# Optimization experiments

Hardware: AMD Instinct MI355X
Metric: run time of the kernel (lower is better)

The kernel has to match this reference:

```python
import math
import jax, jax.numpy as jnp
import numpy as np

B, V, D, H, DE, DFF = 2, 2048, 1024, 16, 256, 4096
DK = D // H


def setup_inputs() -> dict:
    key = jax.random.key(0)
    ks = jax.random.split(key, 24)
    n = lambda k, shape, s=0.02: (jax.random.normal(k, shape, jnp.float32) * s)
    z = lambda *shape: jnp.zeros(shape, jnp.float32)
    return {
        'x': jax.random.normal(ks[0], (B, V, D), jnp.float32),
        'e_node': jax.random.normal(ks[1], (B, V, DE), jnp.float32),
        'conn': jax.random.uniform(ks[2], (B, V, V), jnp.float32),
        'ln1_g': jnp.ones((D,), jnp.float32), 'ln1_b': z(D),
        'f1w1': n(ks[3], (DE, 2 * D)), 'f1b1': z(2 * D),
        'f1w2': n(ks[4], (2 * D, 2 * D)), 'f1b2': z(2 * D),
        'wq': n(ks[5], (D, D)), 'bq': z(D),
        'wk': n(ks[6], (D, D)), 'bk': z(D),
        'wv': n(ks[7], (D, D)), 'bv': z(D),
        'wp': n(ks[8], (D, D)), 'bp': z(D),
        'ln2_g': jnp.ones((D,), jnp.float32), 'ln2_b': z(D),
        'f2w1': n(ks[9], (DE, 2 * D)), 'f2b1': z(2 * D),
        'f2w2': n(ks[10], (2 * D, 2 * D)), 'f2b2': z(2 * D),
        'ffw1': n(ks[11], (D, DFF)), 'ffb1': z(DFF),
        'ffw2': n(ks[12], (DFF, D)), 'ffb2': z(D),
    }


def _ln(x, g, b):
    m = x.mean(-1, keepdims=True)
    v = ((x - m) ** 2).mean(-1, keepdims=True)
    return (x - m) / jnp.sqrt(v + 1e-5) * g + b


def _film(e, w1, b1, w2, b2):
    h = jax.nn.gelu(e @ w1 + b1, approximate=False)  # torch F.gelu default = exact erf
    gb = h @ w2 + b2
    return jnp.split(gb, 2, axis=-1)  # gamma, beta


def reference(x, e_node, conn, ln1_g, ln1_b, f1w1, f1b1, f1w2, f1b2,
              wq, bq, wk, bk, wv, bv, wp, bp, ln2_g, ln2_b,
              f2w1, f2b1, f2w2, f2b2, ffw1, ffb1, ffw2, ffb2):
    b, v, d = x.shape
    # Pre-norm + FiLM 1
    y = _ln(x, ln1_g, ln1_b)
    g1, be1 = _film(e_node, f1w1, f1b1, f1w2, f1b2)
    y = y * (1.0 + g1) + be1
    # Multi-head attention with additive log(conn) mask
    heads = lambda t: t.reshape(b, v, H, DK).transpose(0, 2, 1, 3)  # [B,h,V,dk]
    Q = heads(y @ wq + bq)
    K = heads(y @ wk + bk)
    Vv = heads(y @ wv + bv)
    logits = jnp.einsum('bhqd,bhkd->bhqk', Q, K) / math.sqrt(DK)
    log_mask = jnp.log(jnp.clip(conn, 0.0, 1.0) + 1e-6)[:, None]  # [B,1,V,V]
    s = logits + log_mask
    s = s - s.max(-1, keepdims=True)
    a = jnp.exp(s)
    a = a / (a.sum(-1, keepdims=True) + 1e-8)
    o = jnp.einsum('bhqk,bhkd->bhqd', a, Vv)
    o = o.transpose(0, 2, 1, 3).reshape(b, v, d)
    x = x + (o @ wp + bp)
    # Pre-norm + FiLM 2 + FFN
    y2 = _ln(x, ln2_g, ln2_b)
    g2, be2 = _film(e_node, f2w1, f2b1, f2w2, f2b2)
    y2 = y2 * (1.0 + g2) + be2
    y2 = jax.nn.gelu(y2 @ ffw1 + ffb1, approximate=False) @ ffw2 + ffb2
    return x + y2
```

## Files before the change

kernel.cpp:

```cpp
#include <hip/hip_runtime.h>
#include <math.h>
#include <stdint.h>

#define B_   2
#define V_   2048
#define D_   1024
#define H_   16
#define DK_  64
#define DE_  256
#define DFF_ 4096
#define M_   (B_*V_)
#define D2_  (2*D_)
#define D3_  (3*D_)

typedef unsigned short u16;
typedef unsigned int   u32;
typedef __bf16 bf16x8 __attribute__((ext_vector_type(8)));
typedef u16    u16x8  __attribute__((ext_vector_type(8)));
typedef u16    u16x4  __attribute__((ext_vector_type(4)));
typedef float  f32x4  __attribute__((ext_vector_type(4)));
typedef u32    u32x2  __attribute__((ext_vector_type(2)));
typedef u32    u32x4  __attribute__((ext_vector_type(4)));

__device__ __forceinline__ float bf2f(u16 u) {
    union { unsigned int i; float f; } z; z.i = ((unsigned int)u) << 16; return z.f;
}
__device__ __forceinline__ u16 f2bf(float f) {
    union { float f; unsigned int i; } z; z.f = f;
    unsigned int x = z.i;
    return (u16)((x + 0x7fffu + ((x >> 16) & 1u)) >> 16);
}
__device__ __forceinline__ float gelu_erf(float v) {
    return 0.5f * v * (1.0f + erff(v * 0.70710678118654752f));
}
__device__ __forceinline__ float ldv(const float* p) { return *p; }
__device__ __forceinline__ float ldv(const u16* p)   { return bf2f(*p); }
__device__ __forceinline__ void  stv(float* p, float v) { *p = v; }
__device__ __forceinline__ void  stv(u16* p,   float v) { *p = f2bf(v); }

__device__ __forceinline__ void gload16(const u16* g, u16* lds)
{
    __builtin_amdgcn_global_load_lds(
        (const __attribute__((address_space(1))) void*)g,
        (__attribute__((address_space(3))) void*)(uintptr_t)lds,
        16, 0, 0);
}

__global__ void convT_k(const float* __restrict__ W, u16* __restrict__ Wt, int K, int N)
{
    __shared__ float tile[32][33];
    const int n0 = blockIdx.x * 32, k0 = blockIdx.y * 32;
    const int tx = threadIdx.x, ty = threadIdx.y;
    #pragma unroll
    for (int j = 0; j < 4; ++j)
        tile[ty * 4 + j][tx] = W[(size_t)(k0 + ty * 4 + j) * N + n0 + tx];
    __syncthreads();
    #pragma unroll
    for (int j = 0; j < 4; ++j)
        Wt[(size_t)(n0 + ty * 4 + j) * K + k0 + tx] = f2bf(tile[tx][ty * 4 + j]);
}

__global__ void conv_k(const float* __restrict__ X, u16* __restrict__ Y)
{
    const int i = (blockIdx.x * 256 + threadIdx.x) * 4;
    f32x4 v = *reinterpret_cast<const f32x4*>(X + i);
    u16x4 o;
    #pragma unroll
    for (int j = 0; j < 4; ++j) o[j] = f2bf(v[j]);
    *reinterpret_cast<u16x4*>(Y + i) = o;
}

__global__ void lmask_k(const float* __restrict__ conn, u16* __restrict__ Lm)
{
    const size_t i = ((size_t)blockIdx.x * 256 + threadIdx.x) * 8;
    f32x4 a = *reinterpret_cast<const f32x4*>(conn + i);
    f32x4 b = *reinterpret_cast<const f32x4*>(conn + i + 4);
    u16x8 o;
    #pragma unroll
    for (int j = 0; j < 4; ++j) {
        o[j]     = f2bf(__logf(fminf(fmaxf(a[j], 0.f), 1.f) + 1e-6f));
        o[j + 4] = f2bf(__logf(fminf(fmaxf(b[j], 0.f), 1.f) + 1e-6f));
    }
    *reinterpret_cast<u16x8*>(Lm + i) = o;
}

__global__ void qkvbias_k(const float* __restrict__ bq, const float* __restrict__ bk,
                          const float* __restrict__ bv, float* __restrict__ o)
{
    int i = blockIdx.x * 256 + threadIdx.x;
    o[i] = i < 1024 ? bq[i] : (i < 2048 ? bk[i - 1024] : bv[i - 2048]);
}

template<int EPI, typename TC, typename TRES>
__launch_bounds__(256)
__global__ void gemm_k(const u16* __restrict__ A, const u16* __restrict__ Wt,
                       const float* __restrict__ bias, const TRES* __restrict__ res,
                       TC* __restrict__ C, int M, int N, int K)
{
    __shared__ u16 As[128 * 64];
    __shared__ u16 Bs[128 * 64];

    const int tid  = threadIdx.x;
    const int lane = tid & 63;
    const int w    = tid >> 6;
    const int wm   = (w >> 1) * 64, wn = (w & 1) * 64;
    const int m0   = blockIdx.y * 128, n0 = blockIdx.x * 128;
    const int l15  = lane & 15, l4 = lane >> 4;

    int rr[4], cc[4];
    #pragma unroll
    for (int i = 0; i < 4; ++i) {
        rr[i] = w * 32 + i * 8 + (lane >> 3);
        cc[i] = (lane & 7) ^ (rr[i] & 7);
    }

    f32x4 acc[4][4] = {};

    for (int k0 = 0; k0 < K; k0 += 64) {
        if (k0) __syncthreads();
        #pragma unroll
        for (int i = 0; i < 4; ++i) {
            gload16(A  + (size_t)(m0 + rr[i]) * K + k0 + cc[i] * 8, &As[w * 2048 + i * 512]);
            gload16(Wt + (size_t)(n0 + rr[i]) * K + k0 + cc[i] * 8, &Bs[w * 2048 + i * 512]);
        }
        __syncthreads();

        #pragma unroll
        for (int kk = 0; kk < 2; ++kk) {
            bf16x8 a[4], b[4];
            #pragma unroll
            for (int mb = 0; mb < 4; ++mb) {
                int r  = wm + mb * 16 + l15;
                int ph = (kk * 4 + l4) ^ (r & 7);
                a[mb] = *reinterpret_cast<const bf16x8*>(&As[r * 64 + ph * 8]);
            }
            #pragma unroll
            for (int nb = 0; nb < 4; ++nb) {
                int r  = wn + nb * 16 + l15;
                int ph = (kk * 4 + l4) ^ (r & 7);
                b[nb] = *reinterpret_cast<const bf16x8*>(&Bs[r * 64 + ph * 8]);
            }
            #pragma unroll
            for (int mb = 0; mb < 4; ++mb)
                #pragma unroll
                for (int nb = 0; nb < 4; ++nb)
                    acc[mb][nb] = __builtin_amdgcn_mfma_f32_16x16x32_bf16(a[mb], b[nb], acc[mb][nb], 0, 0, 0);
        }
    }

    #pragma unroll
    for (int nb = 0; nb < 4; ++nb) {
        int col = n0 + wn + nb * 16 + l15;
        float bv = bias[col];
        #pragma unroll
        for (int mb = 0; mb < 4; ++mb) {
            #pragma unroll
            for (int i = 0; i < 4; ++i) {
                int row = m0 + wm + mb * 16 + l4 * 4 + i;
                float v = acc[mb][nb][i] + bv;
                if (EPI == 1) v = gelu_erf(v);
                if (EPI == 2) v += ldv(res + (size_t)row * N + col);
                stv(C + (size_t)row * N + col, v);
            }
        }
    }
}

template<typename TX>
__launch_bounds__(256)
__global__ void lnfilm_k(const TX* __restrict__ X, const u16* __restrict__ GB,
                         const float* __restrict__ g, const float* __restrict__ bb,
                         u16* __restrict__ Y)
{
    const int row = blockIdx.x;
    const int tid = threadIdx.x;
    const TX* xr = X + (size_t)row * D_;
    float xs[4], s = 0.f, sq = 0.f;
    #pragma unroll
    for (int j = 0; j < 4; ++j) {
        float v = ldv(xr + tid + j * 256);
        xs[j] = v; s += v; sq += v * v;
    }
    #pragma unroll
    for (int off = 32; off; off >>= 1) {
        s  += __shfl_xor(s, off);
        sq += __shfl_xor(sq, off);
    }
    __shared__ float rs[4], rq[4];
    const int w = tid >> 6;
    if ((tid & 63) == 0) { rs[w] = s; rq[w] = sq; }
    __syncthreads();
    s  = rs[0] + rs[1] + rs[2] + rs[3];
    sq = rq[0] + rq[1] + rq[2] + rq[3];
    const float mean = s * (1.0f / D_);
    const float var  = sq * (1.0f / D_) - mean * mean;
    const float rstd = rsqrtf(fmaxf(var, 0.f) + 1e-5f);
    const u16* gbr = GB + (size_t)row * D2_;
    #pragma unroll
    for (int j = 0; j < 4; ++j) {
        int d = tid + j * 256;
        float v = (xs[j] - mean) * rstd * g[d] + bb[d];
        v = v * (1.0f + bf2f(gbr[d])) + bf2f(gbr[D_ + d]);
        Y[(size_t)row * D_ + d] = f2bf(v);
    }
}

__launch_bounds__(256)
__global__ void attn_k(const u16* __restrict__ Q, const u16* __restrict__ K,
                       const u16* __restrict__ Vv, const u16* __restrict__ Lm,
                       u16* __restrict__ O, int ld)
{
    __shared__ u16 Ks[64 * 64];
    __shared__ u16 Vs[64 * 64];
    __shared__ u16 Lms[64 * 64];
    __shared__ u16 Ps[4 * 16 * 72];

    const int blk = blockIdx.x;
    const int qt  = blk & 31;
    const int h   = (blk >> 5) & 15;
    const int b   = blk >> 9;
    const int q0  = qt * 64;
    const int tid = threadIdx.x, lane = tid & 63, w = tid >> 6;
    const int l15 = lane & 15, l4 = lane >> 4;
    const size_t bV = (size_t)b * V_;

    const u16* qp = Q + (bV + q0 + w * 16 + l15) * ld + h * 64;
    bf16x8 qa[2];
    {
        u16x8 r0 = *reinterpret_cast<const u16x8*>(qp + l4 * 8);
        u16x8 r1 = *reinterpret_cast<const u16x8*>(qp + 32 + l4 * 8);
        u16x8 s0, s1;
        #pragma unroll
        for (int j = 0; j < 8; ++j) {
            s0[j] = f2bf(bf2f(r0[j]) * 0.125f);
            s1[j] = f2bf(bf2f(r1[j]) * 0.125f);
        }
        union { u16x8 u; bf16x8 h; } c0, c1;
        c0.u = s0; c1.u = s1;
        qa[0] = c0.h; qa[1] = c1.h;
    }

    const int rStage  = (lane >> 3);
    const int kSrcDk  = ((lane & 7) ^ (lane >> 3)) * 8;
    const int vK      = ((lane >> 5) << 2) + ((lane & 7) >> 1);
    const int vDk     = ((lane >> 3) & 3) * 16 + (lane & 1) * 8;
    const int lmSrc   = ((lane & 7) * 8) ^ ((((w << 1) + (lane >> 5)) & 3) * 16);
    const u32 vaddr   = (u32)(uintptr_t)&Vs[0] + (l4 << 10) + (l15 << 3);

    float lr[4] = {0.f, 0.f, 0.f, 0.f};
    f32x4 o[4] = {};

    for (int kt = 0; kt < V_ / 64; ++kt) {
        const int k0 = kt * 64;
        if (kt) __syncthreads();
        #pragma unroll
        for (int i = 0; i < 2; ++i) {
            int r = i * 32 + w * 8 + rStage;
            gload16(K  + (bV + k0 + r) * ld + h * 64 + kSrcDk,           &Ks[i * 2048 + w * 512]);
            int kv = i * 32 + w * 8 + vK;
            gload16(Vv + (bV + k0 + kv) * ld + h * 64 + vDk,             &Vs[i * 2048 + w * 512]);
            gload16(Lm + (bV + q0 + r) * (size_t)V_ + k0 + lmSrc,        &Lms[i * 2048 + w * 512]);
        }
        __syncthreads();

        f32x4 s[4];
        #pragma unroll
        for (int kb = 0; kb < 4; ++kb) {
            int row = (kb * 16 + l15) * 64;
            bf16x8 b0 = *reinterpret_cast<const bf16x8*>(&Ks[row + ((l4 ^ (l15 & 7)) * 8)]);
            bf16x8 b1 = *reinterpret_cast<const bf16x8*>(&Ks[row + (((l4 + 4) ^ (l15 & 7)) * 8)]);
            f32x4 z = {};
            z = __builtin_amdgcn_mfma_f32_16x16x32_bf16(qa[0], b0, z, 0, 0, 0);
            z = __builtin_amdgcn_mfma_f32_16x16x32_bf16(qa[1], b1, z, 0, 0, 0);
            s[kb] = z;
        }
        float rsum[4] = {0.f, 0.f, 0.f, 0.f};
        #pragma unroll
        for (int i = 0; i < 4; ++i) {
            int lrow = (w * 16 + l4 * 4 + i) * 64;
            #pragma unroll
            for (int kb = 0; kb < 4; ++kb) {
                float p = __expf(s[kb][i] + bf2f(Lms[lrow + ((kb ^ l4) * 16 + l15)]));
                rsum[i] += p;
                Ps[(w * 16 + l4 * 4 + i) * 72 + kb * 16 + l15] = f2bf(p);
            }
        }
        #pragma unroll
        for (int i = 0; i < 4; ++i) {
            float v = rsum[i];
            #pragma unroll
            for (int off = 8; off; off >>= 1) v += __shfl_xor(v, off, 16);
            lr[i] += v;
        }
        #pragma unroll
        for (int c2 = 0; c2 < 2; ++c2) {
            bf16x8 pa = *reinterpret_cast<const bf16x8*>(&Ps[(w * 16 + l15) * 72 + c2 * 32 + l4 * 8]);
            u32 a0 = vaddr + c2 * 4096;
            u32x2 t0, t1, t2, t3, t4, t5, t6, t7;
            asm volatile("ds_read_b64_tr_b16 %0, %1"            : "=v"(t0) : "v"(a0));
            asm volatile("ds_read_b64_tr_b16 %0, %1 offset:512" : "=v"(t1) : "v"(a0));
            asm volatile("ds_read_b64_tr_b16 %0, %1 offset:128" : "=v"(t2) : "v"(a0));
            asm volatile("ds_read_b64_tr_b16 %0, %1 offset:640" : "=v"(t3) : "v"(a0));
            asm volatile("ds_read_b64_tr_b16 %0, %1 offset:256" : "=v"(t4) : "v"(a0));
            asm volatile("ds_read_b64_tr_b16 %0, %1 offset:768" : "=v"(t5) : "v"(a0));
            asm volatile("ds_read_b64_tr_b16 %0, %1 offset:384" : "=v"(t6) : "v"(a0));
            asm volatile("ds_read_b64_tr_b16 %0, %1 offset:896" : "=v"(t7) : "v"(a0));
            asm volatile("s_waitcnt lgkmcnt(0)" ::: "memory");
            __builtin_amdgcn_sched_barrier(0);
            union { u32x4 u; bf16x8 h; } vb0, vb1, vb2, vb3;
            vb0.u = (u32x4){t0.x, t0.y, t1.x, t1.y};
            vb1.u = (u32x4){t2.x, t2.y, t3.x, t3.y};
            vb2.u = (u32x4){t4.x, t4.y, t5.x, t5.y};
            vb3.u = (u32x4){t6.x, t6.y, t7.x, t7.y};
            o[0] = __builtin_amdgcn_mfma_f32_16x16x32_bf16(pa, vb0.h, o[0], 0, 0, 0);
            o[1] = __builtin_amdgcn_mfma_f32_16x16x32_bf16(pa, vb1.h, o[1], 0, 0, 0);
            o[2] = __builtin_amdgcn_mfma_f32_16x16x32_bf16(pa, vb2.h, o[2], 0, 0, 0);
            o[3] = __builtin_amdgcn_mfma_f32_16x16x32_bf16(pa, vb3.h, o[3], 0, 0, 0);
        }
    }

    #pragma unroll
    for (int i = 0; i < 4; ++i) {
        float rcp = 1.0f / (lr[i] + 1e-8f);
        int q = q0 + w * 16 + l4 * 4 + i;
        u16* op = O + (bV + q) * D_ + h * 64;
        #pragma unroll
        for (int nb = 0; nb < 4; ++nb)
            op[nb * 16 + l15] = f2bf(o[nb][i] * rcp);
    }
}

extern "C" void kernel_launch(void* const* d_in, const int* in_sizes, int n_in,
                              void* d_out, int out_size, void* d_ws, size_t ws_size,
                              hipStream_t stream)
{
    (void)in_sizes; (void)n_in; (void)out_size; (void)ws_size;
    const float* x    = (const float*)d_in[0];
    const float* e    = (const float*)d_in[1];
    const float* conn = (const float*)d_in[2];
    const float* ln1g = (const float*)d_in[3];
    const float* ln1b = (const float*)d_in[4];
    const float* f1w1 = (const float*)d_in[5];
    const float* f1b1 = (const float*)d_in[6];
    const float* f1w2 = (const float*)d_in[7];
    const float* f1b2 = (const float*)d_in[8];
    const float* wq   = (const float*)d_in[9];
    const float* bq   = (const float*)d_in[10];
    const float* wk   = (const float*)d_in[11];
    const float* bk   = (const float*)d_in[12];
    const float* wv   = (const float*)d_in[13];
    const float* bv   = (const float*)d_in[14];
    const float* wp   = (const float*)d_in[15];
    const float* bp   = (const float*)d_in[16];
    const float* ln2g = (const float*)d_in[17];
    const float* ln2b = (const float*)d_in[18];
    const float* f2w1 = (const float*)d_in[19];
    const float* f2b1 = (const float*)d_in[20];
    const float* f2w2 = (const float*)d_in[21];
    const float* f2b2 = (const float*)d_in[22];
    const float* ffw1 = (const float*)d_in[23];
    const float* ffb1 = (const float*)d_in[24];
    const float* ffw2 = (const float*)d_in[25];
    const float* ffb2 = (const float*)d_in[26];
    float* out = (float*)d_out;

    char* ws = (char*)d_ws;
    const size_t MB = 1u << 20;
    u16*   Lm    = (u16*)(ws + 0);
    u16*   e_bf  = (u16*)(ws + 16 * MB);
    u16*   h     = (u16*)(ws + 18 * MB);
    u16*   wt2   = (u16*)(ws + 34 * MB);
    u16*   wt8   = (u16*)(ws + 36 * MB);
    u16*   gb    = (u16*)(ws + 44 * MB);
    u16*   y     = (u16*)(ws + 60 * MB);
    u16*   wqkvt = (u16*)(ws + 18 * MB);
    u16*   qkv   = (u16*)(ws + 24 * MB);
    float* qkvb  = (float*)(ws + 71 * MB);
    u16*   o     = (u16*)(ws + 48 * MB);
    u16*   xnew  = (u16*)(ws + 64 * MB);
    u16*   h2    = (u16*)(ws + 18 * MB);
    u16*   gb2   = (u16*)(ws + 44 * MB);
    u16*   y2    = (u16*)(ws + 0);
    u16*   ffw1t = (u16*)(ws + 8 * MB);
    u16*   t     = (u16*)(ws + 16 * MB);
    u16*   ffw2t = (u16*)(ws + 48 * MB);

    dim3 blk(256), tblk(32, 8);
    #define CONVT(W, WT, K, N) convT_k<<<dim3((N)/32, (K)/32), tblk, 0, stream>>>(W, WT, K, N)

    conv_k <<<(M_*DE_)/1024, blk, 0, stream>>>(e, e_bf);
    lmask_k<<<(B_*(size_t)V_*V_)/2048, blk, 0, stream>>>(conn, Lm);

    CONVT(f1w1, wt2, DE_, D2_);
    gemm_k<1, u16, u16><<<dim3(D2_/128, M_/128), blk, 0, stream>>>(e_bf, wt2, f1b1, (const u16*)nullptr, h, M_, D2_, DE_);
    CONVT(f1w2, wt8, D2_, D2_);
    gemm_k<0, u16, u16><<<dim3(D2_/128, M_/128), blk, 0, stream>>>(h, wt8, f1b2, (const u16*)nullptr, gb, M_, D2_, D2_);
    lnfilm_k<float><<<M_, blk, 0, stream>>>(x, gb, ln1g, ln1b, y);
    CONVT(wq, wqkvt,                 D_, D_);
    CONVT(wk, wqkvt + 1024 * 1024,   D_, D_);
    CONVT(wv, wqkvt + 2048 * 1024,   D_, D_);
    qkvbias_k<<<D3_/256, blk, 0, stream>>>(bq, bk, bv, qkvb);
    gemm_k<0, u16, u16><<<dim3(D3_/128, M_/128), blk, 0, stream>>>(y, wqkvt, qkvb, (const u16*)nullptr, qkv, M_, D3_, D_);
    attn_k<<<B_*H_*(V_/64), blk, 0, stream>>>(qkv, qkv + 1024, qkv + 2048, Lm, o, D3_);
    CONVT(wp, wt2, D_, D_);
    gemm_k<2, u16, float><<<dim3(D_/128, M_/128), blk, 0, stream>>>(o, wt2, bp, x, xnew, M_, D_, D_);
    CONVT(f2w1, wt2, DE_, D2_);
    gemm_k<1, u16, u16><<<dim3(D2_/128, M_/128), blk, 0, stream>>>(e_bf, wt2, f2b1, (const u16*)nullptr, h2, M_, D2_, DE_);
    CONVT(f2w2, wt8, D2_, D2_);
    gemm_k<0, u16, u16><<<dim3(D2_/128, M_/128), blk, 0, stream>>>(h2, wt8, f2b2, (const u16*)nullptr, gb2, M_, D2_, D2_);
    lnfilm_k<u16><<<M_, blk, 0, stream>>>(xnew, gb2, ln2g, ln2b, y2);
    CONVT(ffw1, ffw1t, D_, DFF_);
    gemm_k<1, u16, u16><<<dim3(DFF_/128, M_/128), blk, 0, stream>>>(y2, ffw1t, ffb1, (const u16*)nullptr, t, M_, DFF_, D_);
    CONVT(ffw2, ffw2t, DFF_, D_);
    gemm_k<2, float, u16><<<dim3(D_/128, M_/128), blk, 0, stream>>>(t, ffw2t, ffb2, xnew, out, M_, D_, DFF_);
    #undef CONVT
}
```

Baseline: 449.2 us.

## Transpose QK MFMA output, vectorize mask/P LDS traffic, use exp2 softmax

The attention kernel swaps the MFMA operands so each lane holds four consecutive keys of one query row. This lets the log-mask be read as one 4-element vector and the probabilities be written as packed bf16 pairs, instead of scalar LDS accesses. The mask is now stored in log2 form and the softmax uses raw v_exp_f32 with a LOG2E FMA, replacing __expf. The row-sum shuffles move out of the key loop into a single reduction at the end, which adds a cross-lane gather to map sums back to the output layout.

```diff
diff --git a/kernel.cpp b/kernel.cpp
--- a/kernel.cpp
+++ b/kernel.cpp
@@ -78,8 +78,8 @@
     u16x8 o;
     #pragma unroll
     for (int j = 0; j < 4; ++j) {
-        o[j]     = f2bf(__logf(fminf(fmaxf(a[j], 0.f), 1.f) + 1e-6f));
-        o[j + 4] = f2bf(__logf(fminf(fmaxf(b[j], 0.f), 1.f) + 1e-6f));
+        o[j]     = f2bf(__log2f(fminf(fmaxf(a[j], 0.f), 1.f) + 1e-6f));
+        o[j + 4] = f2bf(__log2f(fminf(fmaxf(b[j], 0.f), 1.f) + 1e-6f));
     }
     *reinterpret_cast<u16x8*>(Lm + i) = o;
 }
@@ -240,26 +240,35 @@
         qa[0] = c0.h; qa[1] = c1.h;
     }
 
-    const int rStage  = (lane >> 3);
-    const int kSrcDk  = ((lane & 7) ^ (lane >> 3)) * 8;
-    const int vK      = ((lane >> 5) << 2) + ((lane & 7) >> 1);
-    const int vDk     = ((lane >> 3) & 3) * 16 + (lane & 1) * 8;
-    const int lmSrc   = ((lane & 7) * 8) ^ ((((w << 1) + (lane >> 5)) & 3) * 16);
-    const u32 vaddr   = (u32)(uintptr_t)&Vs[0] + (l4 << 10) + (l15 << 3);
-
-    float lr[4] = {0.f, 0.f, 0.f, 0.f};
-    f32x4 o[4] = {};
+    const int rStage = (lane >> 3);
+    const int cSw    = ((lane & 7) ^ rStage) * 8;
+    const int vK     = ((lane >> 5) << 2) + ((lane & 7) >> 1);
+    const int vDk    = ((lane >> 3) & 3) * 16 + (lane & 1) * 8;
+    const u32 vaddr  = (u32)(uintptr_t)&Vs[0] + (l4 << 10) + (l15 << 3);
+
+    const int lmRow  = w * 16 + l15;
+    const u16* lmBase = &Lms[lmRow * 64 + (l4 & 1) * 4];
+    int lmOff[4];
+    #pragma unroll
+    for (int kb = 0; kb < 4; ++kb)
+        lmOff[kb] = ((((kb << 1) | (l4 >> 1)) ^ (lmRow & 7)) << 3);
+
+    u16* psW = &Ps[(w * 16 + l15) * 72 + l4 * 4];
+    const float LOG2E = 1.44269504088896f;
+
+    float lrp = 0.f;
+    f32x4 o4[4] = {};
 
     for (int kt = 0; kt < V_ / 64; ++kt) {
         const int k0 = kt * 64;
         if (kt) __syncthreads();
         #pragma unroll
         for (int i = 0; i < 2; ++i) {
-            int r = i * 32 + w * 8 + rStage;
-            gload16(K  + (bV + k0 + r) * ld + h * 64 + kSrcDk,           &Ks[i * 2048 + w * 512]);
+            int r  = i * 32 + w * 8 + rStage;
             int kv = i * 32 + w * 8 + vK;
-            gload16(Vv + (bV + k0 + kv) * ld + h * 64 + vDk,             &Vs[i * 2048 + w * 512]);
-            gload16(Lm + (bV + q0 + r) * (size_t)V_ + k0 + lmSrc,        &Lms[i * 2048 + w * 512]);
+            gload16(K  + (bV + k0 + r)  * ld + h * 64 + cSw,   &Ks[i * 2048 + w * 512]);
+            gload16(Vv + (bV + k0 + kv) * ld + h * 64 + vDk,   &Vs[i * 2048 + w * 512]);
+            gload16(Lm + (bV + q0 + r) * (size_t)V_ + k0 + cSw, &Lms[i * 2048 + w * 512]);
         }
         __syncthreads();
 
@@ -267,30 +276,31 @@
         #pragma unroll
         for (int kb = 0; kb < 4; ++kb) {
             int row = (kb * 16 + l15) * 64;
-            bf16x8 b0 = *reinterpret_cast<const bf16x8*>(&Ks[row + ((l4 ^ (l15 & 7)) * 8)]);
-            bf16x8 b1 = *reinterpret_cast<const bf16x8*>(&Ks[row + (((l4 + 4) ^ (l15 & 7)) * 8)]);
+            bf16x8 k0f = *reinterpret_cast<const bf16x8*>(&Ks[row + ((l4 ^ (l15 & 7)) * 8)]);
+            bf16x8 k1f = *reinterpret_cast<const bf16x8*>(&Ks[row + (((l4 + 4) ^ (l15 & 7)) * 8)]);
             f32x4 z = {};
-            z = __builtin_amdgcn_mfma_f32_16x16x32_bf16(qa[0], b0, z, 0, 0, 0);
-            z = __builtin_amdgcn_mfma_f32_16x16x32_bf16(qa[1], b1, z, 0, 0, 0);
+            z = __builtin_amdgcn_mfma_f32_16x16x32_bf16(k0f, qa[0], z, 0, 0, 0);
+            z = __builtin_amdgcn_mfma_f32_16x16x32_bf16(k1f, qa[1], z, 0, 0, 0);
             s[kb] = z;
         }
-        float rsum[4] = {0.f, 0.f, 0.f, 0.f};
-        #pragma unroll
-        for (int i = 0; i < 4; ++i) {
-            int lrow = (w * 16 + l4 * 4 + i) * 64;
-            #pragma unroll
-            for (int kb = 0; kb < 4; ++kb) {
-                float p = __expf(s[kb][i] + bf2f(Lms[lrow + ((kb ^ l4) * 16 + l15)]));
-                rsum[i] += p;
-                Ps[(w * 16 + l4 * 4 + i) * 72 + kb * 16 + l15] = f2bf(p);
-            }
-        }
-        #pragma unroll
-        for (int i = 0; i < 4; ++i) {
-            float v = rsum[i];
-            #pragma unroll
-            for (int off = 8; off; off >>= 1) v += __shfl_xor(v, off, 16);
-            lr[i] += v;
+        #pragma unroll
+        for (int kb = 0; kb < 4; ++kb) {
+            u16x4 lm4 = *reinterpret_cast<const u16x4*>(lmBase + lmOff[kb]);
+            float p0, p1, p2, p3;
+            float t0 = fmaf(s[kb][0], LOG2E, bf2f(lm4[0]));
+            float t1 = fmaf(s[kb][1], LOG2E, bf2f(lm4[1]));
+            float t2 = fmaf(s[kb][2], LOG2E, bf2f(lm4[2]));
+            float t3 = fmaf(s[kb][3], LOG2E, bf2f(lm4[3]));
+            asm("v_exp_f32 %0, %1" : "=v"(p0) : "v"(t0));
+            asm("v_exp_f32 %0, %1" : "=v"(p1) : "v"(t1));
+            asm("v_exp_f32 %0, %1" : "=v"(p2) : "v"(t2));
+            asm("v_exp_f32 %0, %1" : "=v"(p3) : "v"(t3));
+            lrp += (p0 + p1) + (p2 + p3);
+            u32 d0, d1;
+            asm("v_cvt_pk_bf16_f32 %0, %1, %2" : "=v"(d0) : "v"(p0), "v"(p1));
+            asm("v_cvt_pk_bf16_f32 %0, %1, %2" : "=v"(d1) : "v"(p2), "v"(p3));
+            u32x2 dd = {d0, d1};
+            *reinterpret_cast<u32x2*>(psW + kb * 16) = dd;
         }
         #pragma unroll
         for (int c2 = 0; c2 < 2; ++c2) {
@@ -312,21 +322,25 @@
             vb1.u = (u32x4){t2.x, t2.y, t3.x, t3.y};
             vb2.u = (u32x4){t4.x, t4.y, t5.x, t5.y};
             vb3.u = (u32x4){t6.x, t6.y, t7.x, t7.y};
-            o[0] = __builtin_amdgcn_mfma_f32_16x16x32_bf16(pa, vb0.h, o[0], 0, 0, 0);
-            o[1] = __builtin_amdgcn_mfma_f32_16x16x32_bf16(pa, vb1.h, o[1], 0, 0, 0);
-            o[2] = __builtin_amdgcn_mfma_f32_16x16x32_bf16(pa, vb2.h, o[2], 0, 0, 0);
-            o[3] = __builtin_amdgcn_mfma_f32_16x16x32_bf16(pa, vb3.h, o[3], 0, 0, 0);
-        }
-    }
-
+            o4[0] = __builtin_amdgcn_mfma_f32_16x16x32_bf16(pa, vb0.h, o4[0], 0, 0, 0);
+            o4[1] = __builtin_amdgcn_mfma_f32_16x16x32_bf16(pa, vb1.h, o4[1], 0, 0, 0);
+            o4[2] = __builtin_amdgcn_mfma_f32_16x16x32_bf16(pa, vb2.h, o4[2], 0, 0, 0);
+            o4[3] = __builtin_amdgcn_mfma_f32_16x16x32_bf16(pa, vb3.h, o4[3], 0, 0, 0);
+        }
+    }
+
+    float v = lrp;
+    v += __shfl_xor(v, 16);
+    v += __shfl_xor(v, 32);
     #pragma unroll
     for (int i = 0; i < 4; ++i) {
-        float rcp = 1.0f / (lr[i] + 1e-8f);
+        float lw = __shfl(v, (lane & 48) | (((lane >> 4) << 2) + i));
+        float rcp = 1.0f / (lw + 1e-8f);
         int q = q0 + w * 16 + l4 * 4 + i;
         u16* op = O + (bV + q) * D_ + h * 64;
         #pragma unroll
         for (int nb = 0; nb < 4; ++nb)
-            op[nb * 16 + l15] = f2bf(o[nb][i] * rcp);
+            op[nb * 16 + l15] = f2bf(o4[nb][i] * rcp);
     }
 }
 
```

New measurement: 421.0 us. 1.07x faster.
